# Optimization experiments

Hardware: AMD Instinct MI355X
Metric: run time of the kernel (lower is better)

The kernel has to match this reference:

```python
import jax, jax.numpy as jnp
import numpy as np
from jax import lax

KSIZE = 7
SIGMA = 5.0
ALPHA = 0.05


def _gaussian_kernel(ksize: int, sigma: float) -> jnp.ndarray:
    # 2D Gaussian, normalized to sum 1, replicated depthwise for 3 channels: (3,1,k,k)
    ax = jnp.arange(ksize, dtype=jnp.float32) - (ksize - 1) / 2.0
    g1 = jnp.exp(-(ax ** 2) / (2.0 * sigma ** 2))
    g2 = jnp.outer(g1, g1)
    g2 = g2 / jnp.sum(g2)
    return jnp.broadcast_to(g2[None, None], (3, 1, ksize, ksize)).astype(jnp.float32)


def _sobel_kernel() -> jnp.ndarray:
    # (2,1,3,3): channel 0 -> Ix, channel 1 -> Iy
    sx = jnp.array([[-1.0, 0.0, 1.0], [-2.0, 0.0, 2.0], [-1.0, 0.0, 1.0]], dtype=jnp.float32)
    sy = sx.T
    return jnp.stack([sx[None], sy[None]], axis=0)  # (2,1,3,3)


def setup_inputs() -> dict:
    key = jax.random.key(0)
    x = jax.random.normal(key, (1, 1, 4096, 4096), dtype=jnp.float32)
    return {"x": x, "sobel_k": _sobel_kernel(), "gauss_k": _gaussian_kernel(KSIZE, SIGMA)}


def _conv(x, k, pad, groups):
    return lax.conv_general_dilated(
        x, k, window_strides=(1, 1), padding=[(pad, pad), (pad, pad)],
        dimension_numbers=("NCHW", "OIHW", "NCHW"), feature_group_count=groups)


def reference(x, sobel_k, gauss_k):
    # ImageGradientsLayer: Sobel conv -> (1,2,H,W)
    g = _conv(x, sobel_k, 1, 1)
    Ix, Iy = g[:, 0:1], g[:, 1:2]
    # ChannelProductLayer -> (1,3,H,W)
    prod = jnp.concatenate([Ix * Ix, Iy * Iy, Ix * Iy], axis=1)
    # SecondMomentMatrixLayer: depthwise Gaussian blur, groups=3
    S = _conv(prod, gauss_k, KSIZE // 2, 3)
    Sxx, Syy, Sxy = S[0, 0], S[0, 1], S[0, 2]
    # CornerResponseLayer: R = det - alpha*trace^2
    tr = Sxx + Syy
    R = (Sxx * Syy - Sxy * Sxy - ALPHA * tr * tr)[None, None]  # (1,1,H,W)
    # NMSLayer: median threshold, 7x7 maxpool (stride 1, pad 3), keep maxima
    med = jnp.median(R)
    Rt = jnp.where(R >= med, R, jnp.float32(0.0))
    mp = lax.reduce_window(Rt, -jnp.inf, lax.max, (1, 1, 7, 7), (1, 1, 1, 1),
                           [(0, 0), (0, 0), (3, 3), (3, 3)])
    out = jnp.where(Rt != mp, jnp.float32(0.0), mp)
    return out
```

## Files before the change

### kernel.cpp

```cpp
#include <hip/hip_runtime.h>
#include <math.h>

#define N_IMG 4096
#define NBC   1024
#define H_OUT 32
#define HR    38

struct W7 { float w[7]; };

__device__ __forceinline__ unsigned f2k(float f) {
    unsigned u = __float_as_uint(f);
    return (u & 0x80000000u) ? ~u : (u | 0x80000000u);
}
__device__ __forceinline__ float k2f(unsigned k) {
    unsigned u = (k & 0x80000000u) ? (k & 0x7fffffffu) : ~k;
    return __uint_as_float(u);
}

__global__ __launch_bounds__(256) void harris_kernel(const float* __restrict__ x,
                                                     float* __restrict__ R,
                                                     unsigned* __restrict__ ghist,
                                                     W7 wp)
{
    __shared__ unsigned histo[4096];
    const int tid = threadIdx.x;
    for (int i = tid; i < 4096; i += 256) histo[i] = 0;
    __syncthreads();

    const int row0 = blockIdx.y * H_OUT;
    const int jc   = blockIdx.x * NBC + tid * 4;
    const float* w = wp.w;

    float xm[12], xc[12], xp[12];
    float hxx[7][4], hyy[7][4], hxy[7][4];

    auto loadrow = [&](int ri, float* d) {
        if ((unsigned)ri < N_IMG) {
            const float* p = x + (size_t)ri * N_IMG;
            float4 v0 = make_float4(0.f,0.f,0.f,0.f), v2 = make_float4(0.f,0.f,0.f,0.f);
            if (jc >= 4) v0 = *(const float4*)(p + jc - 4);
            float4 v1 = *(const float4*)(p + jc);
            if (jc + 4 < N_IMG) v2 = *(const float4*)(p + jc + 4);
            d[0]=v0.x; d[1]=v0.y; d[2]=v0.z; d[3]=v0.w;
            d[4]=v1.x; d[5]=v1.y; d[6]=v1.z; d[7]=v1.w;
            d[8]=v2.x; d[9]=v2.y; d[10]=v2.z; d[11]=v2.w;
        } else {
            #pragma unroll
            for (int t = 0; t < 12; t++) d[t] = 0.f;
        }
    };

    loadrow(row0 - 4, xm);
    loadrow(row0 - 3, xc);

    int curb = -1; unsigned cnt = 0;

    for (int it = 0; it < 6; ++it) {
        #pragma unroll
        for (int k = 0; k < 7; ++k) {
            const int r = it * 7 + k;
            if (r < HR) {
                const int ri = row0 + r - 3;
                loadrow(ri + 1, xp);

                float sxx[4] = {0,0,0,0}, syy[4] = {0,0,0,0}, sxy[4] = {0,0,0,0};
                if ((unsigned)ri < N_IMG) {
                    float dc[12], rd[12];
                    #pragma unroll
                    for (int t = 0; t < 12; t++) {
                        dc[t] = xm[t] + 2.f * xc[t] + xp[t];
                        rd[t] = xp[t] - xm[t];
                    }
                    #pragma unroll
                    for (int t = 0; t < 10; t++) {
                        float ix = dc[t+2] - dc[t];
                        float iy = rd[t] + 2.f * rd[t+1] + rd[t+2];
                        if ((unsigned)(jc - 3 + t) >= N_IMG) { ix = 0.f; iy = 0.f; }
                        float xx = ix*ix, yy = iy*iy, xy = ix*iy;
                        #pragma unroll
                        for (int o = 0; o < 4; o++) {
                            int v = t - o;
                            if (v >= 0 && v < 7) {
                                sxx[o] = fmaf(w[v], xx, sxx[o]);
                                syy[o] = fmaf(w[v], yy, syy[o]);
                                sxy[o] = fmaf(w[v], xy, sxy[o]);
                            }
                        }
                    }
                }
                #pragma unroll
                for (int o = 0; o < 4; o++) {
                    hxx[k][o] = sxx[o]; hyy[k][o] = syy[o]; hxy[k][o] = sxy[o];
                }

                if (r >= 6) {
                    float4 h;
                    float* hp = &h.x;
                    #pragma unroll
                    for (int o = 0; o < 4; o++) {
                        float ax = 0.f, ay = 0.f, az = 0.f;
                        #pragma unroll
                        for (int u = 0; u < 7; u++) {
                            const int s = (k + 1 + u) % 7;
                            ax = fmaf(w[u], hxx[s][o], ax);
                            ay = fmaf(w[u], hyy[s][o], ay);
                            az = fmaf(w[u], hxy[s][o], az);
                        }
                        float tr = ax + ay;
                        hp[o] = ax*ay - az*az - 0.05f*tr*tr;
                    }
                    const int orow = row0 + r - 6;
                    *(float4*)(R + (size_t)orow * N_IMG + jc) = h;
                    #pragma unroll
                    for (int o = 0; o < 4; o++) {
                        int b = (int)(f2k(hp[o]) >> 20);
                        if (b == curb) cnt++;
                        else { if (curb >= 0) atomicAdd(&histo[curb], cnt); curb = b; cnt = 1; }
                    }
                }
                #pragma unroll
                for (int t = 0; t < 12; t++) { xm[t] = xc[t]; xc[t] = xp[t]; }
            }
        }
    }
    if (curb >= 0) atomicAdd(&histo[curb], cnt);
    __syncthreads();
    for (int i = tid; i < 4096; i += 256) {
        unsigned c = histo[i];
        if (c) atomicAdd(&ghist[i], c);
    }
}

__global__ __launch_bounds__(256) void hist_kernel(const float* __restrict__ R,
                                                   unsigned* __restrict__ ghist,
                                                   const unsigned* __restrict__ state,
                                                   unsigned mask, int shift, int bins)
{
    __shared__ unsigned h[2][4096];
    const int tid = threadIdx.x;
    for (int i = tid; i < 8192; i += 256) ((unsigned*)h)[i] = 0;
    __syncthreads();
    const unsigned p1 = state[0], p2 = state[1];
    const bool dual = (p1 != p2);
    const int n4 = (N_IMG * N_IMG) / 4;
    int curb1 = -1; unsigned cnt1 = 0;
    int curb2 = -1; unsigned cnt2 = 0;
    const float4* R4 = (const float4*)R;
    for (int i = blockIdx.x * 256 + tid; i < n4; i += gridDim.x * 256) {
        float4 v = R4[i];
        float vv[4] = {v.x, v.y, v.z, v.w};
        #pragma unroll
        for (int t = 0; t < 4; t++) {
            unsigned k = f2k(vv[t]);
            if ((k & mask) == p1) {
                int b = (int)((k >> shift) & (unsigned)(bins - 1));
                if (b == curb1) cnt1++;
                else { if (cnt1) atomicAdd(&h[0][curb1], cnt1); curb1 = b; cnt1 = 1; }
            }
            if (dual && (k & mask) == p2) {
                int b = (int)((k >> shift) & (unsigned)(bins - 1));
                if (b == curb2) cnt2++;
                else { if (cnt2) atomicAdd(&h[1][curb2], cnt2); curb2 = b; cnt2 = 1; }
            }
        }
    }
    if (cnt1) atomicAdd(&h[0][curb1], cnt1);
    if (cnt2) atomicAdd(&h[1][curb2], cnt2);
    __syncthreads();
    for (int i = tid; i < bins; i += 256) {
        unsigned c0 = h[0][i]; if (c0) atomicAdd(&ghist[i], c0);
        if (dual) { unsigned c1 = h[1][i]; if (c1) atomicAdd(&ghist[4096 + i], c1); }
    }
}

__global__ __launch_bounds__(256) void select_kernel(unsigned* __restrict__ ghist,
                                                     unsigned* __restrict__ state,
                                                     int shift, int bins, int last)
{
    __shared__ unsigned scan[256];
    __shared__ unsigned res_b[2], res_r[2];
    const int tid = threadIdx.x;
    const int per = bins >> 8;
    unsigned p1 = state[0], p2 = state[1];
    unsigned r1 = state[2], r2 = state[3];
    const bool dual = (p1 != p2);

    for (int q = 0; q < 2; q++) {
        const unsigned* h = (q == 1 && dual) ? (ghist + 4096) : ghist;
        const unsigned rank = (q == 0) ? r1 : r2;
        const int base = tid * per;
        unsigned s = 0;
        for (int i = 0; i < per; i++) s += h[base + i];
        scan[tid] = s;
        __syncthreads();
        unsigned v = s;
        #pragma unroll
        for (int off = 1; off < 256; off <<= 1) {
            unsigned t = (tid >= off) ? scan[tid - off] : 0u;
            __syncthreads();
            v += t;
            scan[tid] = v;
            __syncthreads();
        }
        const unsigned excl = v - s;
        if (rank >= excl && rank < v) {
            unsigned rr = rank - excl;
            unsigned b = (unsigned)base;
            for (int i = 0; i < per; i++) {
                unsigned c = h[base + i];
                if (rr < c) { b = (unsigned)(base + i); break; }
                rr -= c;
            }
            res_b[q] = b; res_r[q] = rr;
        }
        __syncthreads();
    }
    if (tid == 0) {
        p1 |= res_b[0] << shift;  r1 = res_r[0];
        p2 |= res_b[1] << shift;  r2 = res_r[1];
        state[0] = p1; state[1] = p2; state[2] = r1; state[3] = r2;
        if (last) {
            float a = k2f(p1), b = k2f(p2);
            ((float*)state)[4] = 0.5f * (a + b);
        }
    }
    __syncthreads();
    for (int i = tid; i < 8192; i += 256) ghist[i] = 0;
}

__global__ __launch_bounds__(256) void init_kernel(unsigned* __restrict__ ghist,
                                                   unsigned* __restrict__ state)
{
    const int tid = threadIdx.x;
    for (int i = tid; i < 8192; i += 256) ghist[i] = 0;
    if (tid == 0) {
        state[0] = 0u; state[1] = 0u;
        state[2] = 8388607u;
        state[3] = 8388608u;
        state[4] = 0u;
    }
}

__global__ __launch_bounds__(256) void nms_kernel(const float* __restrict__ R,
                                                  const unsigned* __restrict__ state,
                                                  float* __restrict__ out)
{
    const int tid  = threadIdx.x;
    const int row0 = blockIdx.y * H_OUT;
    const int jc   = blockIdx.x * NBC + tid * 4;
    const float med = ((const float*)state)[4];

    float hm[7][4], ct[7][4];

    for (int it = 0; it < 6; ++it) {
        #pragma unroll
        for (int k = 0; k < 7; ++k) {
            const int r = it * 7 + k;
            if (r < HR) {
                const int ri = row0 + r - 3;
                float a[12];
                if ((unsigned)ri < N_IMG) {
                    const float* p = R + (size_t)ri * N_IMG;
                    float4 v1 = *(const float4*)(p + jc);
                    a[4] = (v1.x >= med) ? v1.x : 0.f;
                    a[5] = (v1.y >= med) ? v1.y : 0.f;
                    a[6] = (v1.z >= med) ? v1.z : 0.f;
                    a[7] = (v1.w >= med) ? v1.w : 0.f;
                    if (jc >= 4) {
                        float4 v0 = *(const float4*)(p + jc - 4);
                        a[0] = (v0.x >= med) ? v0.x : 0.f;
                        a[1] = (v0.y >= med) ? v0.y : 0.f;
                        a[2] = (v0.z >= med) ? v0.z : 0.f;
                        a[3] = (v0.w >= med) ? v0.w : 0.f;
                    } else { a[0]=a[1]=a[2]=a[3] = -INFINITY; }
                    if (jc + 4 < N_IMG) {
                        float4 v2 = *(const float4*)(p + jc + 4);
                        a[8]  = (v2.x >= med) ? v2.x : 0.f;
                        a[9]  = (v2.y >= med) ? v2.y : 0.f;
                        a[10] = (v2.z >= med) ? v2.z : 0.f;
                        a[11] = (v2.w >= med) ? v2.w : 0.f;
                    } else { a[8]=a[9]=a[10]=a[11] = -INFINITY; }
                } else {
                    #pragma unroll
                    for (int t = 0; t < 12; t++) a[t] = -INFINITY;
                }
                #pragma unroll
                for (int o = 0; o < 4; o++) {
                    float m = a[o+1];
                    #pragma unroll
                    for (int t = 2; t <= 7; t++) m = fmaxf(m, a[o+t]);
                    hm[k][o] = m;
                    ct[k][o] = a[4+o];
                }
                if (r >= 6) {
                    float4 ov;
                    float* op = &ov.x;
                    #pragma unroll
                    for (int o = 0; o < 4; o++) {
                        float m = hm[(k+1) % 7][o];
                        #pragma unroll
                        for (int u = 1; u < 7; u++) m = fmaxf(m, hm[(k+1+u) % 7][o]);
                        float c = ct[(k+4) % 7][o];
                        op[o] = (c != m) ? 0.f : m;
                    }
                    const int orow = row0 + r - 6;
                    *(float4*)(out + (size_t)orow * N_IMG + jc) = ov;
                }
            }
        }
    }
}

extern "C" void kernel_launch(void* const* d_in, const int* in_sizes, int n_in,
                              void* d_out, int out_size, void* d_ws, size_t ws_size,
                              hipStream_t stream)
{
    const float* x = (const float*)d_in[0];
    float* R = (float*)d_ws;
    unsigned* ghist = (unsigned*)((char*)d_ws + (size_t)N_IMG * N_IMG * 4);
    unsigned* state = ghist + 8192;
    float* out = (float*)d_out;

    W7 wp;
    {
        double g[7], s = 0.0;
        for (int i = 0; i < 7; i++) { double ax = (double)i - 3.0; g[i] = exp(-(ax*ax)/50.0); s += g[i]; }
        for (int i = 0; i < 7; i++) wp.w[i] = (float)(g[i] / s);
    }

    dim3 sgrid(N_IMG / NBC, N_IMG / H_OUT);

    init_kernel<<<1, 256, 0, stream>>>(ghist, state);
    harris_kernel<<<sgrid, 256, 0, stream>>>(x, R, ghist, wp);
    select_kernel<<<1, 256, 0, stream>>>(ghist, state, 20, 4096, 0);
    hist_kernel<<<2048, 256, 0, stream>>>(R, ghist, state, 0xFFF00000u, 8, 4096);
    select_kernel<<<1, 256, 0, stream>>>(ghist, state, 8, 4096, 0);
    hist_kernel<<<2048, 256, 0, stream>>>(R, ghist, state, 0xFFFFFF00u, 0, 256);
    select_kernel<<<1, 256, 0, stream>>>(ghist, state, 0, 256, 1);
    nms_kernel<<<sgrid, 256, 0, stream>>>(R, state, out);
}
```

Baseline: 293.6 us.

## Halve row tile height and prefetch next row in harris and NMS kernels

Reduces rows per block from 32 to 16, giving more blocks at the cost of a larger relative halo. Adds one-row-ahead software prefetch of input rows in both the harris and NMS kernels to hide global load latency. Moves the column boundary masking behind a per-thread edge flag so interior threads skip it. Extra register arrays may raise register pressure and lower occupancy.

```diff
diff --git a/kernel.cpp b/kernel.cpp
--- a/kernel.cpp
+++ b/kernel.cpp
@@ -3,8 +3,8 @@
 
 #define N_IMG 4096
 #define NBC   1024
-#define H_OUT 32
-#define HR    38
+#define H_OUT 16
+#define HR    22
 
 struct W7 { float w[7]; };
 
@@ -30,8 +30,9 @@
     const int row0 = blockIdx.y * H_OUT;
     const int jc   = blockIdx.x * NBC + tid * 4;
     const float* w = wp.w;
-
-    float xm[12], xc[12], xp[12];
+    const bool edge = (jc < 4) || (jc + 8 > N_IMG);
+
+    float xm[12], xc[12], xp[12], xn[12];
     float hxx[7][4], hyy[7][4], hxy[7][4];
 
     auto loadrow = [&](int ri, float* d) {
@@ -52,16 +53,17 @@
 
     loadrow(row0 - 4, xm);
     loadrow(row0 - 3, xc);
+    loadrow(row0 - 2, xp);
 
     int curb = -1; unsigned cnt = 0;
 
-    for (int it = 0; it < 6; ++it) {
+    for (int it = 0; it < (HR + 6) / 7; ++it) {
         #pragma unroll
         for (int k = 0; k < 7; ++k) {
             const int r = it * 7 + k;
             if (r < HR) {
                 const int ri = row0 + r - 3;
-                loadrow(ri + 1, xp);
+                loadrow(ri + 2, xn);
 
                 float sxx[4] = {0,0,0,0}, syy[4] = {0,0,0,0}, sxy[4] = {0,0,0,0};
                 if ((unsigned)ri < N_IMG) {
@@ -71,11 +73,20 @@
                         dc[t] = xm[t] + 2.f * xc[t] + xp[t];
                         rd[t] = xp[t] - xm[t];
                     }
+                    float ixv[10], iyv[10];
                     #pragma unroll
                     for (int t = 0; t < 10; t++) {
-                        float ix = dc[t+2] - dc[t];
-                        float iy = rd[t] + 2.f * rd[t+1] + rd[t+2];
-                        if ((unsigned)(jc - 3 + t) >= N_IMG) { ix = 0.f; iy = 0.f; }
+                        ixv[t] = dc[t+2] - dc[t];
+                        iyv[t] = rd[t] + 2.f * rd[t+1] + rd[t+2];
+                    }
+                    if (edge) {
+                        #pragma unroll
+                        for (int t = 0; t < 10; t++)
+                            if ((unsigned)(jc - 3 + t) >= N_IMG) { ixv[t] = 0.f; iyv[t] = 0.f; }
+                    }
+                    #pragma unroll
+                    for (int t = 0; t < 10; t++) {
+                        float ix = ixv[t], iy = iyv[t];
                         float xx = ix*ix, yy = iy*iy, xy = ix*iy;
                         #pragma unroll
                         for (int o = 0; o < 4; o++) {
@@ -119,7 +130,7 @@
                     }
                 }
                 #pragma unroll
-                for (int t = 0; t < 12; t++) { xm[t] = xc[t]; xc[t] = xp[t]; }
+                for (int t = 0; t < 12; t++) { xm[t] = xc[t]; xc[t] = xp[t]; xp[t] = xn[t]; }
             }
         }
     }
@@ -251,39 +262,45 @@
     const float med = ((const float*)state)[4];
 
     float hm[7][4], ct[7][4];
-
-    for (int it = 0; it < 6; ++it) {
+    float a[12], an[12];
+
+    auto loadrowT = [&](int ri, float* d) {
+        if ((unsigned)ri < N_IMG) {
+            const float* p = R + (size_t)ri * N_IMG;
+            float4 v1 = *(const float4*)(p + jc);
+            d[4] = (v1.x >= med) ? v1.x : 0.f;
+            d[5] = (v1.y >= med) ? v1.y : 0.f;
+            d[6] = (v1.z >= med) ? v1.z : 0.f;
+            d[7] = (v1.w >= med) ? v1.w : 0.f;
+            if (jc >= 4) {
+                float4 v0 = *(const float4*)(p + jc - 4);
+                d[0] = (v0.x >= med) ? v0.x : 0.f;
+                d[1] = (v0.y >= med) ? v0.y : 0.f;
+                d[2] = (v0.z >= med) ? v0.z : 0.f;
+                d[3] = (v0.w >= med) ? v0.w : 0.f;
+            } else { d[0]=d[1]=d[2]=d[3] = -INFINITY; }
+            if (jc + 4 < N_IMG) {
+                float4 v2 = *(const float4*)(p + jc + 4);
+                d[8]  = (v2.x >= med) ? v2.x : 0.f;
+                d[9]  = (v2.y >= med) ? v2.y : 0.f;
+                d[10] = (v2.z >= med) ? v2.z : 0.f;
+                d[11] = (v2.w >= med) ? v2.w : 0.f;
+            } else { d[8]=d[9]=d[10]=d[11] = -INFINITY; }
+        } else {
+            #pragma unroll
+            for (int t = 0; t < 12; t++) d[t] = -INFINITY;
+        }
+    };
+
+    loadrowT(row0 - 3, a);
+
+    for (int it = 0; it < (HR + 6) / 7; ++it) {
         #pragma unroll
         for (int k = 0; k < 7; ++k) {
             const int r = it * 7 + k;
             if (r < HR) {
                 const int ri = row0 + r - 3;
-                float a[12];
-                if ((unsigned)ri < N_IMG) {
-                    const float* p = R + (size_t)ri * N_IMG;
-                    float4 v1 = *(const float4*)(p + jc);
-                    a[4] = (v1.x >= med) ? v1.x : 0.f;
-                    a[5] = (v1.y >= med) ? v1.y : 0.f;
-                    a[6] = (v1.z >= med) ? v1.z : 0.f;
-                    a[7] = (v1.w >= med) ? v1.w : 0.f;
-                    if (jc >= 4) {
-                        float4 v0 = *(const float4*)(p + jc - 4);
-                        a[0] = (v0.x >= med) ? v0.x : 0.f;
-                        a[1] = (v0.y >= med) ? v0.y : 0.f;
-                        a[2] = (v0.z >= med) ? v0.z : 0.f;
-                        a[3] = (v0.w >= med) ? v0.w : 0.f;
-                    } else { a[0]=a[1]=a[2]=a[3] = -INFINITY; }
-                    if (jc + 4 < N_IMG) {
-                        float4 v2 = *(const float4*)(p + jc + 4);
-                        a[8]  = (v2.x >= med) ? v2.x : 0.f;
-                        a[9]  = (v2.y >= med) ? v2.y : 0.f;
-                        a[10] = (v2.z >= med) ? v2.z : 0.f;
-                        a[11] = (v2.w >= med) ? v2.w : 0.f;
-                    } else { a[8]=a[9]=a[10]=a[11] = -INFINITY; }
-                } else {
-                    #pragma unroll
-                    for (int t = 0; t < 12; t++) a[t] = -INFINITY;
-                }
+                loadrowT(ri + 1, an);
                 #pragma unroll
                 for (int o = 0; o < 4; o++) {
                     float m = a[o+1];
@@ -306,6 +323,8 @@
                     const int orow = row0 + r - 6;
                     *(float4*)(out + (size_t)orow * N_IMG + jc) = ov;
                 }
+                #pragma unroll
+                for (int t = 0; t < 12; t++) a[t] = an[t];
             }
         }
     }
```

Result: no change. 292.8 us (-0.3%).

## Fuse select passes into last-block epilogues and halve per-thread column width

Applied to the files above, without the earlier changes.

The three single-block select kernels are removed. Their work now runs in the last finishing block of the harris and hist kernels, detected through an atomic counter gate, which cuts three launches and their serialization gaps. Harris and NMS threads now each handle 2 columns instead of 4 with float2 loads, which doubles the block count. NMS also uses shorter row strips and Harris gets occupancy hints. The trade-off is more halo loads per output, plus the risk of a visibility bug in the threadfence-based last-block pattern.

```diff
diff --git a/kernel.cpp b/kernel.cpp
--- a/kernel.cpp
+++ b/kernel.cpp
@@ -2,9 +2,11 @@
 #include <math.h>
 
 #define N_IMG 4096
-#define NBC   1024
+#define NBC   512
 #define H_OUT 32
 #define HR    38
+#define NMS_HOUT 16
+#define NMS_HR   22
 
 struct W7 { float w[7]; };
 
@@ -17,10 +19,95 @@
     return __uint_as_float(u);
 }
 
-__global__ __launch_bounds__(256) void harris_kernel(const float* __restrict__ x,
-                                                     float* __restrict__ R,
-                                                     unsigned* __restrict__ ghist,
-                                                     W7 wp)
+__device__ __forceinline__ void select_body(unsigned* __restrict__ ghist,
+                                            unsigned* __restrict__ state,
+                                            int shift, int bins, int last,
+                                            int tid)
+{
+    __shared__ unsigned scan[256];
+    __shared__ unsigned res_b[2], res_r[2];
+    const int per = bins >> 8;
+    unsigned p1 = state[0], p2 = state[1];
+    unsigned r1 = state[2], r2 = state[3];
+    const bool dual = (p1 != p2);
+
+    for (int q = 0; q < 2; q++) {
+        unsigned* h = (q == 1 && dual) ? (ghist + 4096) : ghist;
+        const unsigned rank = (q == 0) ? r1 : r2;
+        const int base = tid * per;
+        unsigned loc[16];
+        unsigned s = 0;
+        #pragma unroll
+        for (int i = 0; i < 16; i++) {
+            unsigned c = 0u;
+            if (i < per)
+                c = __hip_atomic_load(&h[base + i], __ATOMIC_RELAXED, __HIP_MEMORY_SCOPE_AGENT);
+            loc[i] = c; s += c;
+        }
+        scan[tid] = s;
+        __syncthreads();
+        unsigned v = s;
+        #pragma unroll
+        for (int off = 1; off < 256; off <<= 1) {
+            unsigned t = (tid >= off) ? scan[tid - off] : 0u;
+            __syncthreads();
+            v += t;
+            scan[tid] = v;
+            __syncthreads();
+        }
+        const unsigned excl = v - s;
+        if (rank >= excl && rank < v) {
+            unsigned rr = rank - excl;
+            unsigned b = 0xFFFFFFFFu;
+            #pragma unroll
+            for (int i = 0; i < 16; i++) {
+                if (i < per && b == 0xFFFFFFFFu) {
+                    unsigned c = loc[i];
+                    if (rr < c) b = (unsigned)(base + i);
+                    else rr -= c;
+                }
+            }
+            if (b == 0xFFFFFFFFu) { b = (unsigned)(base + per - 1); rr = 0; }
+            res_b[q] = b; res_r[q] = rr;
+        }
+        __syncthreads();
+    }
+    if (tid == 0) {
+        p1 |= res_b[0] << shift;  r1 = res_r[0];
+        p2 |= res_b[1] << shift;  r2 = res_r[1];
+        state[0] = p1; state[1] = p2; state[2] = r1; state[3] = r2;
+        if (last) {
+            float a = k2f(p1), b = k2f(p2);
+            ((float*)state)[4] = 0.5f * (a + b);
+        }
+    }
+    __syncthreads();
+    for (int i = tid; i < 8192; i += 256) ghist[i] = 0;
+}
+
+__device__ __forceinline__ bool last_block_gate(unsigned* cnt, int tid, unsigned nblocks)
+{
+    __shared__ unsigned lastFlag;
+    __threadfence();
+    __syncthreads();
+    if (tid == 0) {
+        unsigned v = atomicAdd(cnt, 1u);
+        lastFlag = (v == nblocks - 1u) ? 1u : 0u;
+    }
+    __syncthreads();
+    if (lastFlag) {
+        __threadfence();
+        return true;
+    }
+    return false;
+}
+
+__global__ __launch_bounds__(256, 4) void harris_kernel(const float* __restrict__ x,
+                                                        float* __restrict__ R,
+                                                        unsigned* __restrict__ ghist,
+                                                        unsigned* __restrict__ state,
+                                                        unsigned* __restrict__ cnt,
+                                                        W7 wp)
 {
     __shared__ unsigned histo[4096];
     const int tid = threadIdx.x;
@@ -28,32 +115,35 @@
     __syncthreads();
 
     const int row0 = blockIdx.y * H_OUT;
-    const int jc   = blockIdx.x * NBC + tid * 4;
+    const int jc   = blockIdx.x * NBC + tid * 2;
     const float* w = wp.w;
-
-    float xm[12], xc[12], xp[12];
-    float hxx[7][4], hyy[7][4], hxy[7][4];
+    const bool edge = (jc < 4) || (jc + 5 >= N_IMG);
+
+    float xm[10], xc[10], xp[10];
+    float hxx[7][2], hyy[7][2], hxy[7][2];
 
     auto loadrow = [&](int ri, float* d) {
         if ((unsigned)ri < N_IMG) {
             const float* p = x + (size_t)ri * N_IMG;
-            float4 v0 = make_float4(0.f,0.f,0.f,0.f), v2 = make_float4(0.f,0.f,0.f,0.f);
-            if (jc >= 4) v0 = *(const float4*)(p + jc - 4);
-            float4 v1 = *(const float4*)(p + jc);
-            if (jc + 4 < N_IMG) v2 = *(const float4*)(p + jc + 4);
-            d[0]=v0.x; d[1]=v0.y; d[2]=v0.z; d[3]=v0.w;
-            d[4]=v1.x; d[5]=v1.y; d[6]=v1.z; d[7]=v1.w;
-            d[8]=v2.x; d[9]=v2.y; d[10]=v2.z; d[11]=v2.w;
+            float2 v0 = make_float2(0.f, 0.f), v1 = make_float2(0.f, 0.f);
+            float2 v3 = make_float2(0.f, 0.f), v4 = make_float2(0.f, 0.f);
+            if (jc >= 4)            v0 = *(const float2*)(p + jc - 4);
+            if (jc >= 2)            v1 = *(const float2*)(p + jc - 2);
+            float2 v2 = *(const float2*)(p + jc);
+            if (jc + 3 < N_IMG)     v3 = *(const float2*)(p + jc + 2);
+            if (jc + 5 < N_IMG)     v4 = *(const float2*)(p + jc + 4);
+            d[0]=v0.x; d[1]=v0.y; d[2]=v1.x; d[3]=v1.y; d[4]=v2.x; d[5]=v2.y;
+            d[6]=v3.x; d[7]=v3.y; d[8]=v4.x; d[9]=v4.y;
         } else {
             #pragma unroll
-            for (int t = 0; t < 12; t++) d[t] = 0.f;
+            for (int t = 0; t < 10; t++) d[t] = 0.f;
         }
     };
 
     loadrow(row0 - 4, xm);
     loadrow(row0 - 3, xc);
 
-    int curb = -1; unsigned cnt = 0;
+    int curb = -1; unsigned rcnt = 0;
 
     for (int it = 0; it < 6; ++it) {
         #pragma unroll
@@ -63,23 +153,32 @@
                 const int ri = row0 + r - 3;
                 loadrow(ri + 1, xp);
 
-                float sxx[4] = {0,0,0,0}, syy[4] = {0,0,0,0}, sxy[4] = {0,0,0,0};
+                float sxx[2] = {0,0}, syy[2] = {0,0}, sxy[2] = {0,0};
                 if ((unsigned)ri < N_IMG) {
-                    float dc[12], rd[12];
-                    #pragma unroll
-                    for (int t = 0; t < 12; t++) {
-                        dc[t] = xm[t] + 2.f * xc[t] + xp[t];
+                    float dc[10], rd[10];
+                    #pragma unroll
+                    for (int t = 0; t < 10; t++) {
+                        dc[t] = fmaf(2.f, xc[t], xm[t]) + xp[t];
                         rd[t] = xp[t] - xm[t];
                     }
-                    #pragma unroll
-                    for (int t = 0; t < 10; t++) {
-                        float ix = dc[t+2] - dc[t];
-                        float iy = rd[t] + 2.f * rd[t+1] + rd[t+2];
-                        if ((unsigned)(jc - 3 + t) >= N_IMG) { ix = 0.f; iy = 0.f; }
+                    float ixv[8], iyv[8];
+                    #pragma unroll
+                    for (int t = 0; t < 8; t++) {
+                        ixv[t] = dc[t+2] - dc[t];
+                        iyv[t] = fmaf(2.f, rd[t+1], rd[t]) + rd[t+2];
+                    }
+                    if (edge) {
+                        #pragma unroll
+                        for (int t = 0; t < 8; t++)
+                            if ((unsigned)(jc - 3 + t) >= N_IMG) { ixv[t] = 0.f; iyv[t] = 0.f; }
+                    }
+                    #pragma unroll
+                    for (int t = 0; t < 8; t++) {
+                        float ix = ixv[t], iy = iyv[t];
                         float xx = ix*ix, yy = iy*iy, xy = ix*iy;
                         #pragma unroll
-                        for (int o = 0; o < 4; o++) {
-                            int v = t - o;
+                        for (int o = 0; o < 2; o++) {
+                            const int v = t - o;
                             if (v >= 0 && v < 7) {
                                 sxx[o] = fmaf(w[v], xx, sxx[o]);
                                 syy[o] = fmaf(w[v], yy, syy[o]);
@@ -89,15 +188,14 @@
                     }
                 }
                 #pragma unroll
-                for (int o = 0; o < 4; o++) {
+                for (int o = 0; o < 2; o++) {
                     hxx[k][o] = sxx[o]; hyy[k][o] = syy[o]; hxy[k][o] = sxy[o];
                 }
 
                 if (r >= 6) {
-                    float4 h;
-                    float* hp = &h.x;
-                    #pragma unroll
-                    for (int o = 0; o < 4; o++) {
+                    float hp[2];
+                    #pragma unroll
+                    for (int o = 0; o < 2; o++) {
                         float ax = 0.f, ay = 0.f, az = 0.f;
                         #pragma unroll
                         for (int u = 0; u < 7; u++) {
@@ -110,31 +208,37 @@
                         hp[o] = ax*ay - az*az - 0.05f*tr*tr;
                     }
                     const int orow = row0 + r - 6;
-                    *(float4*)(R + (size_t)orow * N_IMG + jc) = h;
-                    #pragma unroll
-                    for (int o = 0; o < 4; o++) {
+                    float2 stv; stv.x = hp[0]; stv.y = hp[1];
+                    *(float2*)(R + (size_t)orow * N_IMG + jc) = stv;
+                    #pragma unroll
+                    for (int o = 0; o < 2; o++) {
                         int b = (int)(f2k(hp[o]) >> 20);
-                        if (b == curb) cnt++;
-                        else { if (curb >= 0) atomicAdd(&histo[curb], cnt); curb = b; cnt = 1; }
+                        if (b == curb) rcnt++;
+                        else { if (curb >= 0) atomicAdd(&histo[curb], rcnt); curb = b; rcnt = 1; }
                     }
                 }
                 #pragma unroll
-                for (int t = 0; t < 12; t++) { xm[t] = xc[t]; xc[t] = xp[t]; }
-            }
-        }
-    }
-    if (curb >= 0) atomicAdd(&histo[curb], cnt);
+                for (int t = 0; t < 10; t++) { xm[t] = xc[t]; xc[t] = xp[t]; }
+            }
+        }
+    }
+    if (curb >= 0) atomicAdd(&histo[curb], rcnt);
     __syncthreads();
     for (int i = tid; i < 4096; i += 256) {
         unsigned c = histo[i];
         if (c) atomicAdd(&ghist[i], c);
     }
+
+    if (last_block_gate(cnt, tid, gridDim.x * gridDim.y))
+        select_body(ghist, state, 20, 4096, 0, tid);
 }
 
 __global__ __launch_bounds__(256) void hist_kernel(const float* __restrict__ R,
                                                    unsigned* __restrict__ ghist,
-                                                   const unsigned* __restrict__ state,
-                                                   unsigned mask, int shift, int bins)
+                                                   unsigned* __restrict__ state,
+                                                   unsigned* __restrict__ cnt,
+                                                   unsigned mask, int shift, int bins,
+                                                   int last)
 {
     __shared__ unsigned h[2][4096];
     const int tid = threadIdx.x;
@@ -171,65 +275,14 @@
         unsigned c0 = h[0][i]; if (c0) atomicAdd(&ghist[i], c0);
         if (dual) { unsigned c1 = h[1][i]; if (c1) atomicAdd(&ghist[4096 + i], c1); }
     }
-}
-
-__global__ __launch_bounds__(256) void select_kernel(unsigned* __restrict__ ghist,
-                                                     unsigned* __restrict__ state,
-                                                     int shift, int bins, int last)
-{
-    __shared__ unsigned scan[256];
-    __shared__ unsigned res_b[2], res_r[2];
-    const int tid = threadIdx.x;
-    const int per = bins >> 8;
-    unsigned p1 = state[0], p2 = state[1];
-    unsigned r1 = state[2], r2 = state[3];
-    const bool dual = (p1 != p2);
-
-    for (int q = 0; q < 2; q++) {
-        const unsigned* h = (q == 1 && dual) ? (ghist + 4096) : ghist;
-        const unsigned rank = (q == 0) ? r1 : r2;
-        const int base = tid * per;
-        unsigned s = 0;
-        for (int i = 0; i < per; i++) s += h[base + i];
-        scan[tid] = s;
-        __syncthreads();
-        unsigned v = s;
-        #pragma unroll
-        for (int off = 1; off < 256; off <<= 1) {
-            unsigned t = (tid >= off) ? scan[tid - off] : 0u;
-            __syncthreads();
-            v += t;
-            scan[tid] = v;
-            __syncthreads();
-        }
-        const unsigned excl = v - s;
-        if (rank >= excl && rank < v) {
-            unsigned rr = rank - excl;
-            unsigned b = (unsigned)base;
-            for (int i = 0; i < per; i++) {
-                unsigned c = h[base + i];
-                if (rr < c) { b = (unsigned)(base + i); break; }
-                rr -= c;
-            }
-            res_b[q] = b; res_r[q] = rr;
-        }
-        __syncthreads();
-    }
-    if (tid == 0) {
-        p1 |= res_b[0] << shift;  r1 = res_r[0];
-        p2 |= res_b[1] << shift;  r2 = res_r[1];
-        state[0] = p1; state[1] = p2; state[2] = r1; state[3] = r2;
-        if (last) {
-            float a = k2f(p1), b = k2f(p2);
-            ((float*)state)[4] = 0.5f * (a + b);
-        }
-    }
-    __syncthreads();
-    for (int i = tid; i < 8192; i += 256) ghist[i] = 0;
+
+    if (last_block_gate(cnt, tid, gridDim.x))
+        select_body(ghist, state, shift, bins, last, tid);
 }
 
 __global__ __launch_bounds__(256) void init_kernel(unsigned* __restrict__ ghist,
-                                                   unsigned* __restrict__ state)
+                                                   unsigned* __restrict__ state,
+                                                   unsigned* __restrict__ cnt)
 {
     const int tid = threadIdx.x;
     for (int i = tid; i < 8192; i += 256) ghist[i] = 0;
@@ -238,54 +291,59 @@
         state[2] = 8388607u;
         state[3] = 8388608u;
         state[4] = 0u;
-    }
-}
-
-__global__ __launch_bounds__(256) void nms_kernel(const float* __restrict__ R,
-                                                  const unsigned* __restrict__ state,
-                                                  float* __restrict__ out)
+        cnt[0] = 0u; cnt[1] = 0u; cnt[2] = 0u;
+    }
+}
+
+__global__ __launch_bounds__(256, 8) void nms_kernel(const float* __restrict__ R,
+                                                     const unsigned* __restrict__ state,
+                                                     float* __restrict__ out)
 {
     const int tid  = threadIdx.x;
-    const int row0 = blockIdx.y * H_OUT;
-    const int jc   = blockIdx.x * NBC + tid * 4;
+    const int row0 = blockIdx.y * NMS_HOUT;
+    const int jc   = blockIdx.x * NBC + tid * 2;
     const float med = ((const float*)state)[4];
 
-    float hm[7][4], ct[7][4];
-
-    for (int it = 0; it < 6; ++it) {
+    float hm[7][2], ct[7][2];
+
+    for (int it = 0; it < 4; ++it) {
         #pragma unroll
         for (int k = 0; k < 7; ++k) {
             const int r = it * 7 + k;
-            if (r < HR) {
+            if (r < NMS_HR) {
                 const int ri = row0 + r - 3;
-                float a[12];
+                float a[10];
                 if ((unsigned)ri < N_IMG) {
                     const float* p = R + (size_t)ri * N_IMG;
-                    float4 v1 = *(const float4*)(p + jc);
-                    a[4] = (v1.x >= med) ? v1.x : 0.f;
-                    a[5] = (v1.y >= med) ? v1.y : 0.f;
-                    a[6] = (v1.z >= med) ? v1.z : 0.f;
-                    a[7] = (v1.w >= med) ? v1.w : 0.f;
+                    float2 v2 = *(const float2*)(p + jc);
+                    a[4] = (v2.x >= med) ? v2.x : 0.f;
+                    a[5] = (v2.y >= med) ? v2.y : 0.f;
                     if (jc >= 4) {
-                        float4 v0 = *(const float4*)(p + jc - 4);
+                        float2 v0 = *(const float2*)(p + jc - 4);
                         a[0] = (v0.x >= med) ? v0.x : 0.f;
                         a[1] = (v0.y >= med) ? v0.y : 0.f;
-                        a[2] = (v0.z >= med) ? v0.z : 0.f;
-                        a[3] = (v0.w >= med) ? v0.w : 0.f;
-                    } else { a[0]=a[1]=a[2]=a[3] = -INFINITY; }
-                    if (jc + 4 < N_IMG) {
-                        float4 v2 = *(const float4*)(p + jc + 4);
-                        a[8]  = (v2.x >= med) ? v2.x : 0.f;
-                        a[9]  = (v2.y >= med) ? v2.y : 0.f;
-                        a[10] = (v2.z >= med) ? v2.z : 0.f;
-                        a[11] = (v2.w >= med) ? v2.w : 0.f;
-                    } else { a[8]=a[9]=a[10]=a[11] = -INFINITY; }
+                    } else { a[0] = a[1] = -INFINITY; }
+                    if (jc >= 2) {
+                        float2 v1 = *(const float2*)(p + jc - 2);
+                        a[2] = (v1.x >= med) ? v1.x : 0.f;
+                        a[3] = (v1.y >= med) ? v1.y : 0.f;
+                    } else { a[2] = a[3] = -INFINITY; }
+                    if (jc + 3 < N_IMG) {
+                        float2 v3 = *(const float2*)(p + jc + 2);
+                        a[6] = (v3.x >= med) ? v3.x : 0.f;
+                        a[7] = (v3.y >= med) ? v3.y : 0.f;
+                    } else { a[6] = a[7] = -INFINITY; }
+                    if (jc + 5 < N_IMG) {
+                        float2 v4 = *(const float2*)(p + jc + 4);
+                        a[8] = (v4.x >= med) ? v4.x : 0.f;
+                        a[9] = (v4.y >= med) ? v4.y : 0.f;
+                    } else { a[8] = a[9] = -INFINITY; }
                 } else {
                     #pragma unroll
-                    for (int t = 0; t < 12; t++) a[t] = -INFINITY;
+                    for (int t = 0; t < 10; t++) a[t] = -INFINITY;
                 }
                 #pragma unroll
-                for (int o = 0; o < 4; o++) {
+                for (int o = 0; o < 2; o++) {
                     float m = a[o+1];
                     #pragma unroll
                     for (int t = 2; t <= 7; t++) m = fmaxf(m, a[o+t]);
@@ -293,10 +351,9 @@
                     ct[k][o] = a[4+o];
                 }
                 if (r >= 6) {
-                    float4 ov;
-                    float* op = &ov.x;
-                    #pragma unroll
-                    for (int o = 0; o < 4; o++) {
+                    float op[2];
+                    #pragma unroll
+                    for (int o = 0; o < 2; o++) {
                         float m = hm[(k+1) % 7][o];
                         #pragma unroll
                         for (int u = 1; u < 7; u++) m = fmaxf(m, hm[(k+1+u) % 7][o]);
@@ -304,7 +361,8 @@
                         op[o] = (c != m) ? 0.f : m;
                     }
                     const int orow = row0 + r - 6;
-                    *(float4*)(out + (size_t)orow * N_IMG + jc) = ov;
+                    float2 ov; ov.x = op[0]; ov.y = op[1];
+                    *(float2*)(out + (size_t)orow * N_IMG + jc) = ov;
                 }
             }
         }
@@ -319,6 +377,7 @@
     float* R = (float*)d_ws;
     unsigned* ghist = (unsigned*)((char*)d_ws + (size_t)N_IMG * N_IMG * 4);
     unsigned* state = ghist + 8192;
+    unsigned* cntb  = state + 16;
     float* out = (float*)d_out;
 
     W7 wp;
@@ -328,14 +387,12 @@
         for (int i = 0; i < 7; i++) wp.w[i] = (float)(g[i] / s);
     }
 
-    dim3 sgrid(N_IMG / NBC, N_IMG / H_OUT);
-
-    init_kernel<<<1, 256, 0, stream>>>(ghist, state);
-    harris_kernel<<<sgrid, 256, 0, stream>>>(x, R, ghist, wp);
-    select_kernel<<<1, 256, 0, stream>>>(ghist, state, 20, 4096, 0);
-    hist_kernel<<<2048, 256, 0, stream>>>(R, ghist, state, 0xFFF00000u, 8, 4096);
-    select_kernel<<<1, 256, 0, stream>>>(ghist, state, 8, 4096, 0);
-    hist_kernel<<<2048, 256, 0, stream>>>(R, ghist, state, 0xFFFFFF00u, 0, 256);
-    select_kernel<<<1, 256, 0, stream>>>(ghist, state, 0, 256, 1);
-    nms_kernel<<<sgrid, 256, 0, stream>>>(R, state, out);
-}
+    dim3 hgrid(N_IMG / NBC, N_IMG / H_OUT);
+    dim3 ngrid(N_IMG / NBC, N_IMG / NMS_HOUT);
+
+    init_kernel<<<1, 256, 0, stream>>>(ghist, state, cntb);
+    harris_kernel<<<hgrid, 256, 0, stream>>>(x, R, ghist, state, cntb + 0, wp);
+    hist_kernel<<<2048, 256, 0, stream>>>(R, ghist, state, cntb + 1, 0xFFF00000u, 8, 4096, 0);
+    hist_kernel<<<2048, 256, 0, stream>>>(R, ghist, state, cntb + 2, 0xFFFFFF00u, 0, 256, 1);
+    nms_kernel<<<ngrid, 256, 0, stream>>>(R, state, out);
+}
```

Result: slower. 684.4 us (+133.1%).

## Fold median selection into consumer kernels, removing single-block select launches

Applied to the files above, without the earlier changes.

Removes the three single-block select kernels and the shared state buffer. Each downstream kernel (hist1, hist2, nms) now recomputes the radix-select prefix from the global histograms at block start, using a redundant per-block scan. Histograms for each pass get separate buffers, so one init clears them all. This cuts three serialized one-block launches and their tails, at the cost of every block re-reading and scanning up to three histograms.

```diff
diff --git a/kernel.cpp b/kernel.cpp
--- a/kernel.cpp
+++ b/kernel.cpp
@@ -5,6 +5,7 @@
 #define NBC   1024
 #define H_OUT 32
 #define HR    38
+#define NPIX  (N_IMG * N_IMG)
 
 struct W7 { float w[7]; };
 
@@ -17,9 +18,76 @@
     return __uint_as_float(u);
 }
 
+struct SelState { unsigned p1, p2, r1, r2; };
+
+template<int BINS>
+__device__ void locate_pair(const unsigned* __restrict__ h0,
+                            const unsigned* __restrict__ h1,
+                            int shift, SelState& s)
+{
+    __shared__ unsigned scan[256];
+    __shared__ unsigned resb[2], resr[2];
+    const int tid = threadIdx.x;
+    const int per = BINS / 256;
+    const bool same = (h0 == h1);
+
+    for (int q = 0; q < 2; q++) {
+        if (q == 1 && same) break;
+        const unsigned* __restrict__ h = q ? h1 : h0;
+        const int base = tid * per;
+        unsigned sum = 0;
+        #pragma unroll
+        for (int i = 0; i < per; i++) sum += h[base + i];
+        __syncthreads();
+        scan[tid] = sum;
+        __syncthreads();
+        unsigned v = sum;
+        #pragma unroll
+        for (int off = 1; off < 256; off <<= 1) {
+            unsigned t = (tid >= off) ? scan[tid - off] : 0u;
+            __syncthreads();
+            v += t;
+            scan[tid] = v;
+            __syncthreads();
+        }
+        const unsigned excl = v - sum;
+        #pragma unroll
+        for (int w = 0; w < 2; w++) {
+            const unsigned rank = w ? s.r2 : s.r1;
+            const bool mine = w ? (same || q == 1) : (q == 0);
+            if (mine && rank >= excl && rank < v) {
+                unsigned rr = rank - excl;
+                for (int i = 0; i < per; i++) {
+                    unsigned c = h[base + i];
+                    if (rr < c) { resb[w] = (unsigned)(base + i); resr[w] = rr; break; }
+                    rr -= c;
+                }
+            }
+        }
+        __syncthreads();
+    }
+    s.p1 |= resb[0] << shift; s.r1 = resr[0];
+    s.p2 |= resb[1] << shift; s.r2 = resr[1];
+}
+
+__device__ __forceinline__ SelState derive0(const unsigned* __restrict__ g0) {
+    SelState s; s.p1 = 0u; s.p2 = 0u;
+    s.r1 = (unsigned)(NPIX / 2 - 1); s.r2 = (unsigned)(NPIX / 2);
+    locate_pair<4096>(g0, g0, 20, s);
+    return s;
+}
+__device__ __forceinline__ void derive1(const unsigned* __restrict__ g1, SelState& s) {
+    const unsigned* h1 = (s.p1 != s.p2) ? (g1 + 4096) : g1;
+    locate_pair<4096>(g1, h1, 8, s);
+}
+__device__ __forceinline__ void derive2(const unsigned* __restrict__ g2, SelState& s) {
+    const unsigned* h1 = (s.p1 != s.p2) ? (g2 + 256) : g2;
+    locate_pair<256>(g2, h1, 0, s);
+}
+
 __global__ __launch_bounds__(256) void harris_kernel(const float* __restrict__ x,
                                                      float* __restrict__ R,
-                                                     unsigned* __restrict__ ghist,
+                                                     unsigned* __restrict__ g0,
                                                      W7 wp)
 {
     __shared__ unsigned histo[4096];
@@ -127,22 +195,25 @@
     __syncthreads();
     for (int i = tid; i < 4096; i += 256) {
         unsigned c = histo[i];
-        if (c) atomicAdd(&ghist[i], c);
-    }
-}
-
-__global__ __launch_bounds__(256) void hist_kernel(const float* __restrict__ R,
-                                                   unsigned* __restrict__ ghist,
-                                                   const unsigned* __restrict__ state,
-                                                   unsigned mask, int shift, int bins)
+        if (c) atomicAdd(&g0[i], c);
+    }
+}
+
+__global__ __launch_bounds__(256) void hist1_kernel(const float* __restrict__ R,
+                                                    const unsigned* __restrict__ g0,
+                                                    unsigned* __restrict__ g1)
 {
     __shared__ unsigned h[2][4096];
     const int tid = threadIdx.x;
-    for (int i = tid; i < 8192; i += 256) ((unsigned*)h)[i] = 0;
-    __syncthreads();
-    const unsigned p1 = state[0], p2 = state[1];
+    for (int i = tid; i < 8192; i += 256) ((unsigned*)h)[i] = 0u;
+
+    SelState s = derive0(g0);
+    const unsigned p1 = s.p1, p2 = s.p2;
     const bool dual = (p1 != p2);
-    const int n4 = (N_IMG * N_IMG) / 4;
+    const unsigned mask = 0xFFF00000u;
+    const int shift = 8;
+
+    const int n4 = NPIX / 4;
     int curb1 = -1; unsigned cnt1 = 0;
     int curb2 = -1; unsigned cnt2 = 0;
     const float4* R4 = (const float4*)R;
@@ -153,12 +224,12 @@
         for (int t = 0; t < 4; t++) {
             unsigned k = f2k(vv[t]);
             if ((k & mask) == p1) {
-                int b = (int)((k >> shift) & (unsigned)(bins - 1));
+                int b = (int)((k >> shift) & 4095u);
                 if (b == curb1) cnt1++;
                 else { if (cnt1) atomicAdd(&h[0][curb1], cnt1); curb1 = b; cnt1 = 1; }
             }
             if (dual && (k & mask) == p2) {
-                int b = (int)((k >> shift) & (unsigned)(bins - 1));
+                int b = (int)((k >> shift) & 4095u);
                 if (b == curb2) cnt2++;
                 else { if (cnt2) atomicAdd(&h[1][curb2], cnt2); curb2 = b; cnt2 = 1; }
             }
@@ -167,88 +238,79 @@
     if (cnt1) atomicAdd(&h[0][curb1], cnt1);
     if (cnt2) atomicAdd(&h[1][curb2], cnt2);
     __syncthreads();
-    for (int i = tid; i < bins; i += 256) {
-        unsigned c0 = h[0][i]; if (c0) atomicAdd(&ghist[i], c0);
-        if (dual) { unsigned c1 = h[1][i]; if (c1) atomicAdd(&ghist[4096 + i], c1); }
-    }
-}
-
-__global__ __launch_bounds__(256) void select_kernel(unsigned* __restrict__ ghist,
-                                                     unsigned* __restrict__ state,
-                                                     int shift, int bins, int last)
-{
-    __shared__ unsigned scan[256];
-    __shared__ unsigned res_b[2], res_r[2];
+    for (int i = tid; i < 4096; i += 256) {
+        unsigned c0 = h[0][i]; if (c0) atomicAdd(&g1[i], c0);
+        if (dual) { unsigned c1 = h[1][i]; if (c1) atomicAdd(&g1[4096 + i], c1); }
+    }
+}
+
+__global__ __launch_bounds__(256) void hist2_kernel(const float* __restrict__ R,
+                                                    const unsigned* __restrict__ g0,
+                                                    const unsigned* __restrict__ g1,
+                                                    unsigned* __restrict__ g2)
+{
+    __shared__ unsigned h[2][256];
     const int tid = threadIdx.x;
-    const int per = bins >> 8;
-    unsigned p1 = state[0], p2 = state[1];
-    unsigned r1 = state[2], r2 = state[3];
+    for (int i = tid; i < 512; i += 256) ((unsigned*)h)[i] = 0u;
+
+    SelState s = derive0(g0);
+    derive1(g1, s);
+    const unsigned p1 = s.p1, p2 = s.p2;
     const bool dual = (p1 != p2);
-
-    for (int q = 0; q < 2; q++) {
-        const unsigned* h = (q == 1 && dual) ? (ghist + 4096) : ghist;
-        const unsigned rank = (q == 0) ? r1 : r2;
-        const int base = tid * per;
-        unsigned s = 0;
-        for (int i = 0; i < per; i++) s += h[base + i];
-        scan[tid] = s;
-        __syncthreads();
-        unsigned v = s;
-        #pragma unroll
-        for (int off = 1; off < 256; off <<= 1) {
-            unsigned t = (tid >= off) ? scan[tid - off] : 0u;
-            __syncthreads();
-            v += t;
-            scan[tid] = v;
-            __syncthreads();
-        }
-        const unsigned excl = v - s;
-        if (rank >= excl && rank < v) {
-            unsigned rr = rank - excl;
-            unsigned b = (unsigned)base;
-            for (int i = 0; i < per; i++) {
-                unsigned c = h[base + i];
-                if (rr < c) { b = (unsigned)(base + i); break; }
-                rr -= c;
-            }
-            res_b[q] = b; res_r[q] = rr;
-        }
-        __syncthreads();
-    }
-    if (tid == 0) {
-        p1 |= res_b[0] << shift;  r1 = res_r[0];
-        p2 |= res_b[1] << shift;  r2 = res_r[1];
-        state[0] = p1; state[1] = p2; state[2] = r1; state[3] = r2;
-        if (last) {
-            float a = k2f(p1), b = k2f(p2);
-            ((float*)state)[4] = 0.5f * (a + b);
-        }
-    }
+    const unsigned mask = 0xFFFFFF00u;
+
+    const int n4 = NPIX / 4;
+    int curb1 = -1; unsigned cnt1 = 0;
+    int curb2 = -1; unsigned cnt2 = 0;
+    const float4* R4 = (const float4*)R;
+    for (int i = blockIdx.x * 256 + tid; i < n4; i += gridDim.x * 256) {
+        float4 v = R4[i];
+        float vv[4] = {v.x, v.y, v.z, v.w};
+        #pragma unroll
+        for (int t = 0; t < 4; t++) {
+            unsigned k = f2k(vv[t]);
+            if ((k & mask) == p1) {
+                int b = (int)(k & 255u);
+                if (b == curb1) cnt1++;
+                else { if (cnt1) atomicAdd(&h[0][curb1], cnt1); curb1 = b; cnt1 = 1; }
+            }
+            if (dual && (k & mask) == p2) {
+                int b = (int)(k & 255u);
+                if (b == curb2) cnt2++;
+                else { if (cnt2) atomicAdd(&h[1][curb2], cnt2); curb2 = b; cnt2 = 1; }
+            }
+        }
+    }
+    if (cnt1) atomicAdd(&h[0][curb1], cnt1);
+    if (cnt2) atomicAdd(&h[1][curb2], cnt2);
     __syncthreads();
-    for (int i = tid; i < 8192; i += 256) ghist[i] = 0;
-}
-
-__global__ __launch_bounds__(256) void init_kernel(unsigned* __restrict__ ghist,
-                                                   unsigned* __restrict__ state)
+    if (tid < 256) {
+        unsigned c0 = h[0][tid]; if (c0) atomicAdd(&g2[tid], c0);
+        if (dual) { unsigned c1 = h[1][tid]; if (c1) atomicAdd(&g2[256 + tid], c1); }
+    }
+}
+
+__global__ __launch_bounds__(256) void init_kernel(unsigned* __restrict__ g)
 {
     const int tid = threadIdx.x;
-    for (int i = tid; i < 8192; i += 256) ghist[i] = 0;
-    if (tid == 0) {
-        state[0] = 0u; state[1] = 0u;
-        state[2] = 8388607u;
-        state[3] = 8388608u;
-        state[4] = 0u;
-    }
+    for (int i = tid; i < 16384; i += 256) g[i] = 0u;
 }
 
 __global__ __launch_bounds__(256) void nms_kernel(const float* __restrict__ R,
-                                                  const unsigned* __restrict__ state,
+                                                  const unsigned* __restrict__ g0,
+                                                  const unsigned* __restrict__ g1,
+                                                  const unsigned* __restrict__ g2,
                                                   float* __restrict__ out)
 {
     const int tid  = threadIdx.x;
+
+    SelState s = derive0(g0);
+    derive1(g1, s);
+    derive2(g2, s);
+    const float med = 0.5f * (k2f(s.p1) + k2f(s.p2));
+
     const int row0 = blockIdx.y * H_OUT;
     const int jc   = blockIdx.x * NBC + tid * 4;
-    const float med = ((const float*)state)[4];
 
     float hm[7][4], ct[7][4];
 
@@ -317,25 +379,23 @@
 {
     const float* x = (const float*)d_in[0];
     float* R = (float*)d_ws;
-    unsigned* ghist = (unsigned*)((char*)d_ws + (size_t)N_IMG * N_IMG * 4);
-    unsigned* state = ghist + 8192;
+    unsigned* g0 = (unsigned*)((char*)d_ws + (size_t)N_IMG * N_IMG * 4);
+    unsigned* g1 = g0 + 4096;
+    unsigned* g2 = g1 + 8192;
     float* out = (float*)d_out;
 
     W7 wp;
     {
-        double g[7], s = 0.0;
-        for (int i = 0; i < 7; i++) { double ax = (double)i - 3.0; g[i] = exp(-(ax*ax)/50.0); s += g[i]; }
-        for (int i = 0; i < 7; i++) wp.w[i] = (float)(g[i] / s);
+        double g[7], sm = 0.0;
+        for (int i = 0; i < 7; i++) { double ax = (double)i - 3.0; g[i] = exp(-(ax*ax)/50.0); sm += g[i]; }
+        for (int i = 0; i < 7; i++) wp.w[i] = (float)(g[i] / sm);
     }
 
     dim3 sgrid(N_IMG / NBC, N_IMG / H_OUT);
 
-    init_kernel<<<1, 256, 0, stream>>>(ghist, state);
-    harris_kernel<<<sgrid, 256, 0, stream>>>(x, R, ghist, wp);
-    select_kernel<<<1, 256, 0, stream>>>(ghist, state, 20, 4096, 0);
-    hist_kernel<<<2048, 256, 0, stream>>>(R, ghist, state, 0xFFF00000u, 8, 4096);
-    select_kernel<<<1, 256, 0, stream>>>(ghist, state, 8, 4096, 0);
-    hist_kernel<<<2048, 256, 0, stream>>>(R, ghist, state, 0xFFFFFF00u, 0, 256);
-    select_kernel<<<1, 256, 0, stream>>>(ghist, state, 0, 256, 1);
-    nms_kernel<<<sgrid, 256, 0, stream>>>(R, state, out);
-}
+    init_kernel<<<1, 256, 0, stream>>>(g0);
+    harris_kernel<<<sgrid, 256, 0, stream>>>(x, R, g0, wp);
+    hist1_kernel<<<2048, 256, 0, stream>>>(R, g0, g1);
+    hist2_kernel<<<2048, 256, 0, stream>>>(R, g0, g1, g2);
+    nms_kernel<<<sgrid, 256, 0, stream>>>(R, g0, g1, g2, out);
+}
```

After: 299.1 us. Within noise of the previous version (+1.9%).
